# Kernel tuning notes

Measured on AMD Instinct MI355X. Metric: run time of the kernel, lower is better.

## Reference

```python
import jax, jax.numpy as jnp
import numpy as np

N = 50000   # nodes
R = 50      # relations
B = 30      # bases
F_IN = 64   # input features
H = 64      # hidden channels
C = 8       # classes
E = 1000000 # edges


def setup_inputs() -> dict:
    key = jax.random.key(0)
    ks = jax.random.split(key, 16)
    x = jax.random.normal(ks[0], (N, F_IN), jnp.float32)
    edge_index = jax.random.randint(ks[1], (2, E), 0, N)
    edge_type = jax.random.randint(ks[2], (E,), 0, R)
    inp = {"x": x, "edge_index": edge_index, "edge_type": edge_type}
    dims = [(F_IN, H), (H, H), (H, C)]
    i = 3
    for l, (din, dout) in enumerate(dims):
        s = 1.0 / np.sqrt(din)
        inp[f"bases{l}"] = jax.random.normal(ks[i], (B, din, dout), jnp.float32) * s; i += 1
        inp[f"comp{l}"] = jax.random.normal(ks[i], (R, B), jnp.float32) / np.sqrt(B); i += 1
        inp[f"root{l}"] = jax.random.normal(ks[i], (din, dout), jnp.float32) * s; i += 1
        inp[f"bias{l}"] = jnp.zeros((dout,), jnp.float32); i += 1
    return inp


def _rgcn(x, bases, comp, root, bias, src, seg):
    # Per-relation mean aggregation (PyG RGCNConv default aggr='mean'):
    # segment id = dst * R + relation. Mean of source features per (dst, rel),
    # then basis-decomposed transform (linearity lets transform follow the mean).
    din = x.shape[1]
    sums = jax.ops.segment_sum(x[src], seg, num_segments=N * R)          # [N*R, din]
    cnt = jax.ops.segment_sum(jnp.ones((seg.shape[0],), x.dtype), seg, num_segments=N * R)
    inv = jnp.where(cnt > 0, 1.0 / jnp.maximum(cnt, 1.0), 0.0)
    agg = (sums * inv[:, None]).reshape(N, R, din)                        # [N, R, din]
    t = jnp.einsum('nri,rb->nbi', agg, comp)                              # [N, B, din]
    msg = jnp.einsum('nbi,bio->no', t, bases)                             # [N, dout]
    return msg + x @ root + bias


def reference(x, edge_index, edge_type,
              bases0, comp0, root0, bias0,
              bases1, comp1, root1, bias1,
              bases2, comp2, root2, bias2):
    src, dst = edge_index[0], edge_index[1]
    seg = dst * R + edge_type
    params = [(bases0, comp0, root0, bias0),
              (bases1, comp1, root1, bias1),
              (bases2, comp2, root2, bias2)]
    x1 = x
    for b, c, r, bi in params:
        x1 = _rgcn(x, b, c, r, bi, src, seg)
        x = jax.nn.relu(x1)
    # original returns log_softmax of the last conv's pre-ReLU output
    return jax.nn.log_softmax(x1, axis=1)
```

## Files before the change

### kernel.cpp

```cpp
#include <hip/hip_runtime.h>
#include <hip/hip_bf16.h>
#include <hip/hip_fp16.h>
#include <stdint.h>

#define NN   50000
#define RR   50
#define BB   30
#define DIN  64
#define EE   1000000
#define KTOT (BB*DIN + DIN)
#define NBW  16
#define ROWE (KTOT + 8)
#define CPAD 32
#define EPAD (EE + 8*NN + 32)

typedef __attribute__((ext_vector_type(8))) short short8;
typedef __attribute__((ext_vector_type(4))) float floatx4;

#define RFL(x) __builtin_amdgcn_readfirstlane(x)


__global__ void k_hist(const int* __restrict__ dst, const int* __restrict__ et,
                       int* __restrict__ cnt) {
    int e = blockIdx.x * 256 + threadIdx.x;
    if (e < EE) {
        int d = dst[e], r = et[e];
        atomicAdd(&cnt[d * RR + r], 1);
    }
}

__global__ void k_scan1(const int* __restrict__ cnt, int* __restrict__ dcount,
                        int* __restrict__ doff, int* __restrict__ bsum) {
    __shared__ int sh[256];
    int t = threadIdx.x;
    int i = blockIdx.x * 256 + t;
    int vp = 0;
    if (i < NN) {
        const int* c = cnt + (size_t)i * RR;
        int v = 0;
#pragma unroll
        for (int r = 0; r < RR; ++r) v += c[r];
        vp = (v + 7) & ~7;
        dcount[i] = vp;
    }
    sh[t] = vp;
    __syncthreads();
    for (int s = 1; s < 256; s <<= 1) {
        int add = (t >= s) ? sh[t - s] : 0;
        __syncthreads();
        sh[t] += add;
        __syncthreads();
    }
    int incl = sh[t];
    if (i < NN) doff[i] = incl - vp;
    if (t == 255) bsum[blockIdx.x] = incl;
}

__global__ void k_scan2(int* __restrict__ bsum, int nbv) {
    __shared__ int sh[256];
    int t = threadIdx.x;
    int v = (t < nbv) ? bsum[t] : 0;
    sh[t] = v;
    __syncthreads();
    for (int s = 1; s < 256; s <<= 1) {
        int add = (t >= s) ? sh[t - s] : 0;
        __syncthreads();
        sh[t] += add;
        __syncthreads();
    }
    if (t < nbv) bsum[t] = sh[t] - v;
}

__global__ void k_scan3(int* __restrict__ doff, const int* __restrict__ bsum) {
    int i = blockIdx.x * 256 + threadIdx.x;
    if (i < NN) doff[i] += bsum[blockIdx.x];
}

__global__ void k_scatter(const int* __restrict__ src, const int* __restrict__ dst,
                          const int* __restrict__ et, const int* __restrict__ cnt,
                          const int* __restrict__ doff, int* __restrict__ cursor,
                          int2* __restrict__ ep2) {
    int e = blockIdx.x * 256 + threadIdx.x;
    if (e < EE) {
        int d = dst[e], r = et[e], s = src[e];
        int p = doff[d] + atomicAdd(&cursor[d], 1);
        float a = 1.0f / (float)cnt[d * RR + r];
        ep2[p] = make_int2(s | (r << 16), __float_as_int(a));
    }
}


__global__ void k_deghist(const int* __restrict__ dcount, int* __restrict__ dbin) {
    __shared__ int lh[256];
    int t = threadIdx.x;
    int i = blockIdx.x * 256 + t;
    lh[t] = 0;
    __syncthreads();
    if (i < NN) {
        int d = dcount[i]; d = (d > 255) ? 255 : d;
        atomicAdd(&lh[255 - d], 1);
    }
    __syncthreads();
    if (lh[t]) atomicAdd(&dbin[t], lh[t]);
}

__global__ void k_degscan(int* __restrict__ dbin) {
    __shared__ int sh[256];
    int t = threadIdx.x;
    int v = dbin[t];
    sh[t] = v;
    __syncthreads();
    for (int s = 1; s < 256; s <<= 1) {
        int add = (t >= s) ? sh[t - s] : 0;
        __syncthreads();
        sh[t] += add;
        __syncthreads();
    }
    dbin[t] = sh[t] - v;
}

__global__ void k_degscatter(const int* __restrict__ dcount, const int* __restrict__ dbin,
                             int* __restrict__ dcur, int* __restrict__ order) {
    __shared__ int lh[256], lbase[256];
    int t = threadIdx.x;
    int i = blockIdx.x * 256 + t;
    lh[t] = 0;
    __syncthreads();
    int b = 0, lpos = 0;
    if (i < NN) {
        int d = dcount[i]; d = (d > 255) ? 255 : d;
        b = 255 - d;
        lpos = atomicAdd(&lh[b], 1);
    }
    __syncthreads();
    lbase[t] = lh[t] ? atomicAdd(&dcur[t], lh[t]) : 0;
    __syncthreads();
    if (i < NN) order[dbin[b] + lbase[b] + lpos] = i;
}

__global__ void k_cast_x(const float* __restrict__ x, __hip_bfloat16* __restrict__ h) {
    int i = blockIdx.x * 256 + threadIdx.x;
    if (i < NN * DIN / 4) {
        float4 v = reinterpret_cast<const float4*>(x)[i];
        ushort4 o;
        o.x = (ushort)(__bfloat16_as_ushort(__float2bfloat16(v.x)));
        o.y = (ushort)(__bfloat16_as_ushort(__float2bfloat16(v.y)));
        o.z = (ushort)(__bfloat16_as_ushort(__float2bfloat16(v.z)));
        o.w = (ushort)(__bfloat16_as_ushort(__float2bfloat16(v.w)));
        reinterpret_cast<ushort4*>(h)[i] = o;
    }
}

__global__ void k_prep_comp3(const float* __restrict__ c0, const float* __restrict__ c1,
                             const float* __restrict__ c2, __half* __restrict__ cp) {
    int idx = blockIdx.x * 256 + threadIdx.x;
    if (idx < 3 * RR * CPAD) {
        int l = idx / (RR * CPAD);
        int rem = idx - l * (RR * CPAD);
        int r = rem / CPAD, i = rem - r * CPAD;
        const float* c = (l == 0) ? c0 : (l == 1) ? c1 : c2;
        cp[idx] = (i < BB) ? __float2half(c[r * BB + i]) : __float2half(0.f);
    }
}

__global__ void k_prep_w3(const float* __restrict__ b0, const float* __restrict__ r0,
                          const float* __restrict__ b1, const float* __restrict__ r1,
                          const float* __restrict__ b2, const float* __restrict__ r2,
                          short* __restrict__ wt) {
    int idx = blockIdx.x * 256 + threadIdx.x;
    if (idx >= 144 * KTOT) return;
    int row = idx / KTOT, k = idx - row * KTOT;
    const float* bs; const float* rt; int o, dout;
    if (row < 64)       { bs = b0; rt = r0; o = row;        dout = 64; }
    else if (row < 128) { bs = b1; rt = r1; o = row - 64;   dout = 64; }
    else                { bs = b2; rt = r2; o = row - 128;  dout = 8;  }
    float v = 0.f;
    if (o < dout)
        v = (k < BB * DIN) ? bs[k * dout + o] : rt[(k - BB * DIN) * dout + o];
    __hip_bfloat16 hb = __float2bfloat16(v);
    wt[idx] = *reinterpret_cast<const short*>(&hb);
}


#define LOADR8(u, R0, R1, R2, R3) do {                                          \
    const int _u = ((u) < nit) ? (u) : (nit - 1);                               \
    R0 = rec4[4 * _u];     R1 = rec4[4 * _u + 1];                               \
    R2 = rec4[4 * _u + 2]; R3 = rec4[4 * _u + 3];                               \
} while (0)

#define GATH1(sx) ((unsigned)xin16[((sx) & 0xFFFF) * DIN + lane])

#define EDGE_FMA1(_sx, _ai, _g) do {                                            \
    const int4* _cr = (const int4*)(compH + ((unsigned)(_sx) >> 16) * CPAD);    \
    int4 _m0 = _cr[0], _m1 = _cr[1], _m2 = _cr[2], _m3 = _cr[3];                \
    const float _xvf = __uint_as_float((unsigned)(_g) << 16) * __int_as_float(_ai); \
    const __half _xh = __float2half(_xvf);                                      \
    const __half2 _xv2 = __halves2half2(_xh, _xh);                              \
    const __half2* _p0 = reinterpret_cast<const __half2*>(&_m0);                \
    const __half2* _p1 = reinterpret_cast<const __half2*>(&_m1);                \
    const __half2* _p2 = reinterpret_cast<const __half2*>(&_m2);                \
    const __half2* _p3 = reinterpret_cast<const __half2*>(&_m3);                \
    acc[0]  = __hfma2(_p0[0], _xv2, acc[0]);                                    \
    acc[1]  = __hfma2(_p0[1], _xv2, acc[1]);                                    \
    acc[2]  = __hfma2(_p0[2], _xv2, acc[2]);                                    \
    acc[3]  = __hfma2(_p0[3], _xv2, acc[3]);                                    \
    acc[4]  = __hfma2(_p1[0], _xv2, acc[4]);                                    \
    acc[5]  = __hfma2(_p1[1], _xv2, acc[5]);                                    \
    acc[6]  = __hfma2(_p1[2], _xv2, acc[6]);                                    \
    acc[7]  = __hfma2(_p1[3], _xv2, acc[7]);                                    \
    acc[8]  = __hfma2(_p2[0], _xv2, acc[8]);                                    \
    acc[9]  = __hfma2(_p2[1], _xv2, acc[9]);                                    \
    acc[10] = __hfma2(_p2[2], _xv2, acc[10]);                                   \
    acc[11] = __hfma2(_p2[3], _xv2, acc[11]);                                   \
    acc[12] = __hfma2(_p3[0], _xv2, acc[12]);                                   \
    acc[13] = __hfma2(_p3[1], _xv2, acc[13]);                                   \
    acc[14] = __hfma2(_p3[2], _xv2, acc[14]);                                   \
    acc[15] = __hfma2(_p3[3], _xv2, acc[15]);                                   \
} while (0)

template <int DOUT, bool RELU>
__global__ __launch_bounds__(1024, 8)
void k_fused(const __hip_bfloat16* __restrict__ xin,
             const int2* __restrict__ ep2,
             const int* __restrict__ doff, const int* __restrict__ dcount,
             const int* __restrict__ order,
             const __half* __restrict__ compH,
             const short* __restrict__ Wt,
             const float* __restrict__ bias,
             void* __restrict__ outp) {
    __shared__ __align__(16) char smem_raw[NBW * ROWE * 2];
    auto t_tile = reinterpret_cast<__hip_bfloat16(*)[ROWE]>(smem_raw);
    const unsigned short* xin16 = reinterpret_cast<const unsigned short*>(xin);
    const int tid  = threadIdx.x;
    const int lane = tid & 63;
    const int wv   = RFL(tid >> 6);
    const int node0 = blockIdx.x * NBW;

    {
        const int j = wv;
        const int n = RFL(order[node0 + j]);
        __half2 acc[16];
#pragma unroll
        for (int u = 0; u < 16; ++u)
            acc[u] = __halves2half2(__float2half(0.f), __float2half(0.f));
        const int beg = RFL(doff[n]);
        const int nit = RFL(dcount[n]) >> 3;
        const unsigned selfb = (unsigned)xin16[n * DIN + lane];

        if (nit > 0) {
            const int4* rec4 = (const int4*)(ep2 + beg);
            int4 A0, A1, A2, A3, B0, B1, B2, B3, C0, C1, C2, C3;
            LOADR8(0, A0, A1, A2, A3);
            LOADR8(1, B0, B1, B2, B3);
            unsigned g0 = GATH1(RFL(A0.x)), g1 = GATH1(RFL(A0.z));
            unsigned g2 = GATH1(RFL(A1.x)), g3 = GATH1(RFL(A1.z));
            unsigned g4 = GATH1(RFL(A2.x)), g5 = GATH1(RFL(A2.z));
            unsigned g6 = GATH1(RFL(A3.x)), g7 = GATH1(RFL(A3.z));

            for (int t = 0; t < nit; ++t) {
                unsigned h0 = GATH1(RFL(B0.x)), h1 = GATH1(RFL(B0.z));
                unsigned h2 = GATH1(RFL(B1.x)), h3 = GATH1(RFL(B1.z));
                unsigned h4 = GATH1(RFL(B2.x)), h5 = GATH1(RFL(B2.z));
                unsigned h6 = GATH1(RFL(B3.x)), h7 = GATH1(RFL(B3.z));
                EDGE_FMA1(RFL(A0.x), RFL(A0.y), g0);
                EDGE_FMA1(RFL(A0.z), RFL(A0.w), g1);
                EDGE_FMA1(RFL(A1.x), RFL(A1.y), g2);
                EDGE_FMA1(RFL(A1.z), RFL(A1.w), g3);
                EDGE_FMA1(RFL(A2.x), RFL(A2.y), g4);
                EDGE_FMA1(RFL(A2.z), RFL(A2.w), g5);
                EDGE_FMA1(RFL(A3.x), RFL(A3.y), g6);
                EDGE_FMA1(RFL(A3.z), RFL(A3.w), g7);
                __builtin_amdgcn_sched_barrier(0);
                LOADR8(t + 2, C0, C1, C2, C3);
                A0 = B0; A1 = B1; A2 = B2; A3 = B3;
                B0 = C0; B1 = C1; B2 = C2; B3 = C3;
                g0 = h0; g1 = h1; g2 = h2; g3 = h3;
                g4 = h4; g5 = h5; g6 = h6; g7 = h7;
            }
        }
#pragma unroll
        for (int b = 0; b < BB; ++b) {
            const float v = (b & 1) ? __high2float(acc[b >> 1]) : __low2float(acc[b >> 1]);
            t_tile[j][b * DIN + lane] = __float2bfloat16(v);
        }
        t_tile[j][BB * DIN + lane] =
            __float2bfloat16(__uint_as_float(selfb << 16));
    }
    __syncthreads();

    const int m = lane & 15;
    const int q = lane >> 4;
    int kk0, nsteps, col_base, kpart;
    if (DOUT == 64) {
        kpart = wv >> 2;
        col_base = (wv & 3) * 16;
        kk0    = (kpart <= 1) ? kpart * 16 : (kpart == 2 ? 32 : 47);
        nsteps = (kpart <= 1) ? 16 : 15;
    } else {
        kpart = wv;
        col_base = 0;
        kk0    = (kpart < 14) ? kpart * 4 : (kpart == 14 ? 56 : 59);
        nsteps = (kpart < 14) ? 4 : 3;
    }
    const __hip_bfloat16* arow = &t_tile[m][q * 8];
    const short* brow = Wt + (size_t)(col_base + m) * KTOT + q * 8;

    floatx4 acc0 = {0.f, 0.f, 0.f, 0.f};
    floatx4 acc1 = {0.f, 0.f, 0.f, 0.f};
    int s = 0;
    for (; s + 2 <= nsteps; s += 2) {
        const int kk = kk0 + s;
        short8 a0 = *reinterpret_cast<const short8*>(arow + kk * 32);
        short8 b0 = *reinterpret_cast<const short8*>(brow + kk * 32);
        short8 a1 = *reinterpret_cast<const short8*>(arow + (kk + 1) * 32);
        short8 b1 = *reinterpret_cast<const short8*>(brow + (kk + 1) * 32);
        acc0 = __builtin_amdgcn_mfma_f32_16x16x32_bf16(a0, b0, acc0, 0, 0, 0);
        acc1 = __builtin_amdgcn_mfma_f32_16x16x32_bf16(a1, b1, acc1, 0, 0, 0);
    }
    if (s < nsteps) {
        const int kk = kk0 + s;
        short8 a0 = *reinterpret_cast<const short8*>(arow + kk * 32);
        short8 b0 = *reinterpret_cast<const short8*>(brow + kk * 32);
        acc0 = __builtin_amdgcn_mfma_f32_16x16x32_bf16(a0, b0, acc0, 0, 0, 0);
    }
    floatx4 P = acc0 + acc1;

    __syncthreads();
    float* red = (float*)smem_raw;

    if (DOUT == 64) {
        if (kpart > 0) {
            const int slot = (wv & 3) * 3 + (kpart - 1);
            const int off = (slot * 64 + lane) * 6;
            red[off] = P[0]; red[off + 1] = P[1]; red[off + 2] = P[2]; red[off + 3] = P[3];
        }
        __syncthreads();
        if (kpart == 0) {
#pragma unroll
            for (int t = 0; t < 3; ++t) {
                const int off = (((wv & 3) * 3 + t) * 64 + lane) * 6;
                P[0] += red[off]; P[1] += red[off + 1];
                P[2] += red[off + 2]; P[3] += red[off + 3];
            }
            const int o = col_base + m;
            const float bi = bias[o];
#pragma unroll
            for (int r = 0; r < 4; ++r) {
                const int n = order[node0 + q * 4 + r];
                float v = P[r] + bi;
                if (RELU) {
                    v = fmaxf(v, 0.f);
                    reinterpret_cast<__hip_bfloat16*>(outp)[(size_t)n * DOUT + o] =
                        __float2bfloat16(v);
                } else {
                    reinterpret_cast<float*>(outp)[(size_t)n * DOUT + o] = v;
                }
            }
        }
    } else {
        if (kpart > 0) {
            const int off = ((kpart - 1) * 64 + lane) * 6;
            red[off] = P[0]; red[off + 1] = P[1]; red[off + 2] = P[2]; red[off + 3] = P[3];
        }
        __syncthreads();
        if (kpart == 0) {
#pragma unroll
            for (int w = 0; w < 15; ++w) {
                const int off = (w * 64 + lane) * 6;
                P[0] += red[off]; P[1] += red[off + 1];
                P[2] += red[off + 2]; P[3] += red[off + 3];
            }
            if (m < DOUT) {
                const int o = m;
                const float bi = bias[o];
#pragma unroll
                for (int r = 0; r < 4; ++r) {
                    const int n = order[node0 + q * 4 + r];
                    reinterpret_cast<float*>(outp)[(size_t)n * DOUT + o] = P[r] + bi;
                }
            }
        }
    }
}

__global__ void k_lsm(const float* __restrict__ pre, float* __restrict__ out) {
    int n = blockIdx.x * 256 + threadIdx.x;
    if (n < NN) {
        float v[8];
        float mx = -1e30f;
#pragma unroll
        for (int c = 0; c < 8; ++c) { v[c] = pre[n * 8 + c]; mx = fmaxf(mx, v[c]); }
        float s = 0.f;
#pragma unroll
        for (int c = 0; c < 8; ++c) s += expf(v[c] - mx);
        float ls = logf(s);
#pragma unroll
        for (int c = 0; c < 8; ++c) out[n * 8 + c] = v[c] - mx - ls;
    }
}

extern "C" void kernel_launch(void* const* d_in, const int* in_sizes, int n_in,
                              void* d_out, int out_size, void* d_ws, size_t ws_size,
                              hipStream_t stream) {
    const float* x     = (const float*)d_in[0];
    const int*   eidx  = (const int*)d_in[1];
    const int*   etype = (const int*)d_in[2];
    const float* bases0 = (const float*)d_in[3];
    const float* comp0  = (const float*)d_in[4];
    const float* root0  = (const float*)d_in[5];
    const float* bias0  = (const float*)d_in[6];
    const float* bases1 = (const float*)d_in[7];
    const float* comp1  = (const float*)d_in[8];
    const float* root1  = (const float*)d_in[9];
    const float* bias1  = (const float*)d_in[10];
    const float* bases2 = (const float*)d_in[11];
    const float* comp2  = (const float*)d_in[12];
    const float* root2  = (const float*)d_in[13];
    const float* bias2  = (const float*)d_in[14];
    const int* srcp = eidx;
    const int* dstp = eidx + EE;

    char* p = (char*)d_ws;
    auto carve = [&](size_t bytes) -> char* {
        char* r = p;
        p += (bytes + 255) & ~(size_t)255;
        return r;
    };
    int*  cnt    = (int*)carve((size_t)NN * RR * sizeof(int));
    int*  dcount = (int*)carve((size_t)NN * sizeof(int));
    int*  cursor = (int*)carve((size_t)NN * sizeof(int));
    int*  doff   = (int*)carve((size_t)NN * sizeof(int));
    int*  bsum   = (int*)carve(256 * sizeof(int));
    int*  dbin   = (int*)carve(256 * sizeof(int));
    int*  dcur   = (int*)carve(256 * sizeof(int));
    int*  order  = (int*)carve((size_t)NN * sizeof(int));
    int2* ep2    = (int2*)carve((size_t)EPAD * sizeof(int2));
    __hip_bfloat16* h0 = (__hip_bfloat16*)carve((size_t)NN * DIN * 2);
    __hip_bfloat16* h1 = (__hip_bfloat16*)carve((size_t)NN * DIN * 2);
    __hip_bfloat16* h2 = (__hip_bfloat16*)carve((size_t)NN * DIN * 2);
    float* pre = (float*)carve((size_t)NN * 8 * sizeof(float));
    short* wtA = (short*)carve((size_t)144 * KTOT * sizeof(short));
    __half* cpA = (__half*)carve((size_t)3 * RR * CPAD * sizeof(__half));

    hipMemsetAsync(cnt, 0, (size_t)NN * (RR + 2) * sizeof(int) + 512, stream);
    hipMemsetAsync(dbin, 0, 2048, stream);
    hipMemsetAsync(ep2, 0, (size_t)EPAD * sizeof(int2), stream);

    const int EB = (EE + 255) / 256;
    const int NB = (NN + 255) / 256;
    k_hist<<<EB, 256, 0, stream>>>(dstp, etype, cnt);
    k_scan1<<<NB, 256, 0, stream>>>(cnt, dcount, doff, bsum);
    k_scan2<<<1, 256, 0, stream>>>(bsum, NB);
    k_scan3<<<NB, 256, 0, stream>>>(doff, bsum);
    k_scatter<<<EB, 256, 0, stream>>>(srcp, dstp, etype, cnt, doff, cursor, ep2);
    k_deghist<<<NB, 256, 0, stream>>>(dcount, dbin);
    k_degscan<<<1, 256, 0, stream>>>(dbin);
    k_degscatter<<<NB, 256, 0, stream>>>(dcount, dbin, dcur, order);
    k_cast_x<<<(NN * DIN / 4 + 255) / 256, 256, 0, stream>>>(x, h0);
    k_prep_comp3<<<(3 * RR * CPAD + 255) / 256, 256, 0, stream>>>(comp0, comp1, comp2, cpA);
    k_prep_w3<<<(144 * KTOT + 255) / 256, 256, 0, stream>>>(bases0, root0, bases1, root1,
                                                            bases2, root2, wtA);

    short* wt0 = wtA;
    short* wt1 = wtA + (size_t)64 * KTOT;
    short* wt2 = wtA + (size_t)128 * KTOT;
    __half* cp0 = cpA;
    __half* cp1 = cpA + RR * CPAD;
    __half* cp2 = cpA + 2 * RR * CPAD;

    const int NF = NN / NBW;
    k_fused<64, true ><<<NF, 1024, 0, stream>>>(h0, ep2, doff, dcount, order, cp0, wt0, bias0, (void*)h1);
    k_fused<64, true ><<<NF, 1024, 0, stream>>>(h1, ep2, doff, dcount, order, cp1, wt1, bias1, (void*)h2);
    k_fused<8,  false><<<NF, 1024, 0, stream>>>(h2, ep2, doff, dcount, order, cp2, wt2, bias2, (void*)pre);
    k_lsm<<<NB, 256, 0, stream>>>(pre, (float*)d_out);
}
```

Measured before the change: 557.0 us.

## Quantize node features to int8 with per-row scales and pack edge records

Node activations are stored as int8 with a per-node scale in place of bf16, which halves the bytes per gathered feature. Edge records shrink from 8 to 4 bytes by packing the segment count into the upper bits, with its reciprocal read from a shared-memory table. Per-edge accumulation now uses fp32 vector FMA instead of fp16 half2. The layer epilogue computes a row max through shared atomics and writes quantized outputs, which adds a synchronisation and an extra per-edge scale load, and risks accuracy loss from int8 activations.

```diff
diff --git a/kernel.cpp b/kernel.cpp
--- a/kernel.cpp
+++ b/kernel.cpp
@@ -1,6 +1,5 @@
 #include <hip/hip_runtime.h>
 #include <hip/hip_bf16.h>
-#include <hip/hip_fp16.h>
 #include <stdint.h>
 
 #define NN   50000
@@ -79,13 +78,13 @@
 __global__ void k_scatter(const int* __restrict__ src, const int* __restrict__ dst,
                           const int* __restrict__ et, const int* __restrict__ cnt,
                           const int* __restrict__ doff, int* __restrict__ cursor,
-                          int2* __restrict__ ep2) {
+                          int* __restrict__ ep) {
     int e = blockIdx.x * 256 + threadIdx.x;
     if (e < EE) {
         int d = dst[e], r = et[e], s = src[e];
         int p = doff[d] + atomicAdd(&cursor[d], 1);
-        float a = 1.0f / (float)cnt[d * RR + r];
-        ep2[p] = make_int2(s | (r << 16), __float_as_int(a));
+        int c = cnt[d * RR + r]; c = (c > 255) ? 255 : c;
+        ep[p] = s | (r << 16) | (c << 22);
     }
 }
 
@@ -138,28 +137,30 @@
     if (i < NN) order[dbin[b] + lbase[b] + lpos] = i;
 }
 
-__global__ void k_cast_x(const float* __restrict__ x, __hip_bfloat16* __restrict__ h) {
-    int i = blockIdx.x * 256 + threadIdx.x;
-    if (i < NN * DIN / 4) {
-        float4 v = reinterpret_cast<const float4*>(x)[i];
-        ushort4 o;
-        o.x = (ushort)(__bfloat16_as_ushort(__float2bfloat16(v.x)));
-        o.y = (ushort)(__bfloat16_as_ushort(__float2bfloat16(v.y)));
-        o.z = (ushort)(__bfloat16_as_ushort(__float2bfloat16(v.z)));
-        o.w = (ushort)(__bfloat16_as_ushort(__float2bfloat16(v.w)));
-        reinterpret_cast<ushort4*>(h)[i] = o;
+__global__ void k_quant_x(const float* __restrict__ x, signed char* __restrict__ xq,
+                          float* __restrict__ xs) {
+    const int wv = threadIdx.x >> 6, lane = threadIdx.x & 63;
+    const int n = blockIdx.x * 4 + wv;
+    if (n < NN) {
+        float v = x[n * DIN + lane];
+        float av = fabsf(v);
+#pragma unroll
+        for (int s = 32; s; s >>= 1) av = fmaxf(av, __shfl_xor(av, s));
+        const float inv = (av > 0.f) ? 127.f / av : 0.f;
+        xq[n * DIN + lane] = (signed char)(int)rintf(v * inv);
+        if (lane == 0) xs[n] = av * (1.f / 127.f);
     }
 }
 
 __global__ void k_prep_comp3(const float* __restrict__ c0, const float* __restrict__ c1,
-                             const float* __restrict__ c2, __half* __restrict__ cp) {
+                             const float* __restrict__ c2, float* __restrict__ cp) {
     int idx = blockIdx.x * 256 + threadIdx.x;
     if (idx < 3 * RR * CPAD) {
         int l = idx / (RR * CPAD);
         int rem = idx - l * (RR * CPAD);
         int r = rem / CPAD, i = rem - r * CPAD;
         const float* c = (l == 0) ? c0 : (l == 1) ? c1 : c2;
-        cp[idx] = (i < BB) ? __float2half(c[r * BB + i]) : __float2half(0.f);
+        cp[idx] = (i < BB) ? c[r * BB + i] : 0.f;
     }
 }
 
@@ -182,109 +183,91 @@
 }
 
 
-#define LOADR8(u, R0, R1, R2, R3) do {                                          \
+#define LOADR8(u, RA, RB) do {                                                  \
     const int _u = ((u) < nit) ? (u) : (nit - 1);                               \
-    R0 = rec4[4 * _u];     R1 = rec4[4 * _u + 1];                               \
-    R2 = rec4[4 * _u + 2]; R3 = rec4[4 * _u + 3];                               \
+    RA = rec4[2 * _u]; RB = rec4[2 * _u + 1];                                   \
 } while (0)
 
-#define GATH1(sx) ((unsigned)xin16[((sx) & 0xFFFF) * DIN + lane])
-
-#define EDGE_FMA1(_sx, _ai, _g) do {                                            \
-    const int4* _cr = (const int4*)(compH + ((unsigned)(_sx) >> 16) * CPAD);    \
-    int4 _m0 = _cr[0], _m1 = _cr[1], _m2 = _cr[2], _m3 = _cr[3];                \
-    const float _xvf = __uint_as_float((unsigned)(_g) << 16) * __int_as_float(_ai); \
-    const __half _xh = __float2half(_xvf);                                      \
-    const __half2 _xv2 = __halves2half2(_xh, _xh);                              \
-    const __half2* _p0 = reinterpret_cast<const __half2*>(&_m0);                \
-    const __half2* _p1 = reinterpret_cast<const __half2*>(&_m1);                \
-    const __half2* _p2 = reinterpret_cast<const __half2*>(&_m2);                \
-    const __half2* _p3 = reinterpret_cast<const __half2*>(&_m3);                \
-    acc[0]  = __hfma2(_p0[0], _xv2, acc[0]);                                    \
-    acc[1]  = __hfma2(_p0[1], _xv2, acc[1]);                                    \
-    acc[2]  = __hfma2(_p0[2], _xv2, acc[2]);                                    \
-    acc[3]  = __hfma2(_p0[3], _xv2, acc[3]);                                    \
-    acc[4]  = __hfma2(_p1[0], _xv2, acc[4]);                                    \
-    acc[5]  = __hfma2(_p1[1], _xv2, acc[5]);                                    \
-    acc[6]  = __hfma2(_p1[2], _xv2, acc[6]);                                    \
-    acc[7]  = __hfma2(_p1[3], _xv2, acc[7]);                                    \
-    acc[8]  = __hfma2(_p2[0], _xv2, acc[8]);                                    \
-    acc[9]  = __hfma2(_p2[1], _xv2, acc[9]);                                    \
-    acc[10] = __hfma2(_p2[2], _xv2, acc[10]);                                   \
-    acc[11] = __hfma2(_p2[3], _xv2, acc[11]);                                   \
-    acc[12] = __hfma2(_p3[0], _xv2, acc[12]);                                   \
-    acc[13] = __hfma2(_p3[1], _xv2, acc[13]);                                   \
-    acc[14] = __hfma2(_p3[2], _xv2, acc[14]);                                   \
-    acc[15] = __hfma2(_p3[3], _xv2, acc[15]);                                   \
+#define GATH1(sx) ((int)xss[((sx) & 0xFFFF) * DIN + lane])
+
+#define EDGE_FMA1(_sx, _gi) do {                                                \
+    const int _c = ((_sx) >> 22) & 255;                                         \
+    const float _sc = xscale[(_sx) & 0xFFFF];                                   \
+    const float _a = _sc * rcpl[_c];                                            \
+    const floatx4* _q = (const floatx4*)(compP + (((_sx) >> 16) & 63) * CPAD);  \
+    const float _xv = (float)(_gi) * _a;                                        \
+    const floatx4 _w = {_xv, _xv, _xv, _xv};                                    \
+    acc[0] = _q[0] * _w + acc[0];  acc[1] = _q[1] * _w + acc[1];                \
+    acc[2] = _q[2] * _w + acc[2];  acc[3] = _q[3] * _w + acc[3];                \
+    acc[4] = _q[4] * _w + acc[4];  acc[5] = _q[5] * _w + acc[5];                \
+    acc[6] = _q[6] * _w + acc[6];  acc[7] = _q[7] * _w + acc[7];                \
 } while (0)
 
 template <int DOUT, bool RELU>
 __global__ __launch_bounds__(1024, 8)
-void k_fused(const __hip_bfloat16* __restrict__ xin,
-             const int2* __restrict__ ep2,
+void k_fused(const signed char* __restrict__ xss,
+             const float* __restrict__ xscale,
+             const int* __restrict__ ep,
              const int* __restrict__ doff, const int* __restrict__ dcount,
              const int* __restrict__ order,
-             const __half* __restrict__ compH,
+             const float* __restrict__ compP,
              const short* __restrict__ Wt,
              const float* __restrict__ bias,
-             void* __restrict__ outp) {
+             void* __restrict__ outp,
+             float* __restrict__ oscale) {
     __shared__ __align__(16) char smem_raw[NBW * ROWE * 2];
+    __shared__ float rcpl[256];
     auto t_tile = reinterpret_cast<__hip_bfloat16(*)[ROWE]>(smem_raw);
-    const unsigned short* xin16 = reinterpret_cast<const unsigned short*>(xin);
     const int tid  = threadIdx.x;
     const int lane = tid & 63;
     const int wv   = RFL(tid >> 6);
     const int node0 = blockIdx.x * NBW;
 
+    if (tid < 256) rcpl[tid] = (tid == 0) ? 0.f : (1.0f / (float)tid);
+
+    const int n   = RFL(order[node0 + wv]);
+    const int beg = RFL(doff[n]);
+    const int nit = RFL(dcount[n]) >> 3;
+    const int selfq = GATH1(n);
+    const float sscale = RFL(__float_as_int(xscale[n])) == 0 ? 0.f : xscale[n];
+
+    __syncthreads();
+
     {
-        const int j = wv;
-        const int n = RFL(order[node0 + j]);
-        __half2 acc[16];
-#pragma unroll
-        for (int u = 0; u < 16; ++u)
-            acc[u] = __halves2half2(__float2half(0.f), __float2half(0.f));
-        const int beg = RFL(doff[n]);
-        const int nit = RFL(dcount[n]) >> 3;
-        const unsigned selfb = (unsigned)xin16[n * DIN + lane];
+        floatx4 acc[8];
+#pragma unroll
+        for (int u = 0; u < 8; ++u) acc[u] = (floatx4){0.f, 0.f, 0.f, 0.f};
 
         if (nit > 0) {
-            const int4* rec4 = (const int4*)(ep2 + beg);
-            int4 A0, A1, A2, A3, B0, B1, B2, B3, C0, C1, C2, C3;
-            LOADR8(0, A0, A1, A2, A3);
-            LOADR8(1, B0, B1, B2, B3);
-            unsigned g0 = GATH1(RFL(A0.x)), g1 = GATH1(RFL(A0.z));
-            unsigned g2 = GATH1(RFL(A1.x)), g3 = GATH1(RFL(A1.z));
-            unsigned g4 = GATH1(RFL(A2.x)), g5 = GATH1(RFL(A2.z));
-            unsigned g6 = GATH1(RFL(A3.x)), g7 = GATH1(RFL(A3.z));
+            const int4* rec4 = (const int4*)(ep + beg);
+            int4 A0, A1, B0, B1, C0, C1;
+            LOADR8(0, A0, A1);
+            LOADR8(1, B0, B1);
+            int g0 = GATH1(RFL(A0.x)), g1 = GATH1(RFL(A0.y));
+            int g2 = GATH1(RFL(A0.z)), g3 = GATH1(RFL(A0.w));
+            int g4 = GATH1(RFL(A1.x)), g5 = GATH1(RFL(A1.y));
+            int g6 = GATH1(RFL(A1.z)), g7 = GATH1(RFL(A1.w));
 
             for (int t = 0; t < nit; ++t) {
-                unsigned h0 = GATH1(RFL(B0.x)), h1 = GATH1(RFL(B0.z));
-                unsigned h2 = GATH1(RFL(B1.x)), h3 = GATH1(RFL(B1.z));
-                unsigned h4 = GATH1(RFL(B2.x)), h5 = GATH1(RFL(B2.z));
-                unsigned h6 = GATH1(RFL(B3.x)), h7 = GATH1(RFL(B3.z));
-                EDGE_FMA1(RFL(A0.x), RFL(A0.y), g0);
-                EDGE_FMA1(RFL(A0.z), RFL(A0.w), g1);
-                EDGE_FMA1(RFL(A1.x), RFL(A1.y), g2);
-                EDGE_FMA1(RFL(A1.z), RFL(A1.w), g3);
-                EDGE_FMA1(RFL(A2.x), RFL(A2.y), g4);
-                EDGE_FMA1(RFL(A2.z), RFL(A2.w), g5);
-                EDGE_FMA1(RFL(A3.x), RFL(A3.y), g6);
-                EDGE_FMA1(RFL(A3.z), RFL(A3.w), g7);
+                int h0 = GATH1(RFL(B0.x)), h1 = GATH1(RFL(B0.y));
+                int h2 = GATH1(RFL(B0.z)), h3 = GATH1(RFL(B0.w));
+                int h4 = GATH1(RFL(B1.x)), h5 = GATH1(RFL(B1.y));
+                int h6 = GATH1(RFL(B1.z)), h7 = GATH1(RFL(B1.w));
+                EDGE_FMA1(RFL(A0.x), g0); EDGE_FMA1(RFL(A0.y), g1);
+                EDGE_FMA1(RFL(A0.z), g2); EDGE_FMA1(RFL(A0.w), g3);
+                EDGE_FMA1(RFL(A1.x), g4); EDGE_FMA1(RFL(A1.y), g5);
+                EDGE_FMA1(RFL(A1.z), g6); EDGE_FMA1(RFL(A1.w), g7);
                 __builtin_amdgcn_sched_barrier(0);
-                LOADR8(t + 2, C0, C1, C2, C3);
-                A0 = B0; A1 = B1; A2 = B2; A3 = B3;
-                B0 = C0; B1 = C1; B2 = C2; B3 = C3;
+                LOADR8(t + 2, C0, C1);
+                A0 = B0; A1 = B1; B0 = C0; B1 = C1;
                 g0 = h0; g1 = h1; g2 = h2; g3 = h3;
                 g4 = h4; g5 = h5; g6 = h6; g7 = h7;
             }
         }
 #pragma unroll
-        for (int b = 0; b < BB; ++b) {
-            const float v = (b & 1) ? __high2float(acc[b >> 1]) : __low2float(acc[b >> 1]);
-            t_tile[j][b * DIN + lane] = __float2bfloat16(v);
-        }
-        t_tile[j][BB * DIN + lane] =
-            __float2bfloat16(__uint_as_float(selfb << 16));
+        for (int b = 0; b < BB; ++b)
+            t_tile[wv][b * DIN + lane] = __float2bfloat16(acc[b >> 2][b & 3]);
+        t_tile[wv][BB * DIN + lane] = __float2bfloat16((float)selfq * sscale);
     }
     __syncthreads();
 
@@ -327,6 +310,7 @@
 
     __syncthreads();
     float* red = (float*)smem_raw;
+    float* rowmax = (float*)(smem_raw + 20480);
 
     if (DOUT == 64) {
         if (kpart > 0) {
@@ -334,7 +318,9 @@
             const int off = (slot * 64 + lane) * 6;
             red[off] = P[0]; red[off + 1] = P[1]; red[off + 2] = P[2]; red[off + 3] = P[3];
         }
-        __syncthreads();
+        if (tid < 16) ((int*)rowmax)[tid] = 0;
+        __syncthreads();
+        float vr[4];
         if (kpart == 0) {
 #pragma unroll
             for (int t = 0; t < 3; ++t) {
@@ -346,15 +332,23 @@
             const float bi = bias[o];
 #pragma unroll
             for (int r = 0; r < 4; ++r) {
-                const int n = order[node0 + q * 4 + r];
-                float v = P[r] + bi;
-                if (RELU) {
-                    v = fmaxf(v, 0.f);
-                    reinterpret_cast<__hip_bfloat16*>(outp)[(size_t)n * DOUT + o] =
-                        __float2bfloat16(v);
-                } else {
-                    reinterpret_cast<float*>(outp)[(size_t)n * DOUT + o] = v;
-                }
+                const float v = fmaxf(P[r] + bi, 0.f);
+                vr[r] = v;
+                atomicMax((int*)&rowmax[q * 4 + r], __float_as_int(v));
+            }
+        }
+        __syncthreads();
+        if (kpart == 0) {
+            const int o = col_base + m;
+#pragma unroll
+            for (int r = 0; r < 4; ++r) {
+                const int slot2 = q * 4 + r;
+                const float mx = rowmax[slot2];
+                const float inv = (mx > 0.f) ? 127.f / mx : 0.f;
+                const int nw = order[node0 + slot2];
+                reinterpret_cast<signed char*>(outp)[(size_t)nw * 64 + o] =
+                    (signed char)(int)rintf(vr[r] * inv);
+                if (wv == 0 && m == 0) oscale[nw] = mx * (1.f / 127.f);
             }
         }
     } else {
@@ -375,8 +369,8 @@
                 const float bi = bias[o];
 #pragma unroll
                 for (int r = 0; r < 4; ++r) {
-                    const int n = order[node0 + q * 4 + r];
-                    reinterpret_cast<float*>(outp)[(size_t)n * DOUT + o] = P[r] + bi;
+                    const int nw = order[node0 + q * 4 + r];
+                    reinterpret_cast<float*>(outp)[(size_t)nw * DOUT + o] = P[r] + bi;
                 }
             }
         }
@@ -434,17 +428,18 @@
     int*  dbin   = (int*)carve(256 * sizeof(int));
     int*  dcur   = (int*)carve(256 * sizeof(int));
     int*  order  = (int*)carve((size_t)NN * sizeof(int));
-    int2* ep2    = (int2*)carve((size_t)EPAD * sizeof(int2));
-    __hip_bfloat16* h0 = (__hip_bfloat16*)carve((size_t)NN * DIN * 2);
-    __hip_bfloat16* h1 = (__hip_bfloat16*)carve((size_t)NN * DIN * 2);
-    __hip_bfloat16* h2 = (__hip_bfloat16*)carve((size_t)NN * DIN * 2);
+    int*  ep     = (int*)carve((size_t)EPAD * sizeof(int));
+    signed char* xqA = (signed char*)carve((size_t)NN * DIN);
+    signed char* xqB = (signed char*)carve((size_t)NN * DIN);
+    float* xsA = (float*)carve((size_t)NN * sizeof(float));
+    float* xsB = (float*)carve((size_t)NN * sizeof(float));
     float* pre = (float*)carve((size_t)NN * 8 * sizeof(float));
     short* wtA = (short*)carve((size_t)144 * KTOT * sizeof(short));
-    __half* cpA = (__half*)carve((size_t)3 * RR * CPAD * sizeof(__half));
+    float* cpA = (float*)carve((size_t)3 * RR * CPAD * sizeof(float));
 
     hipMemsetAsync(cnt, 0, (size_t)NN * (RR + 2) * sizeof(int) + 512, stream);
     hipMemsetAsync(dbin, 0, 2048, stream);
-    hipMemsetAsync(ep2, 0, (size_t)EPAD * sizeof(int2), stream);
+    hipMemsetAsync(ep, 0, (size_t)EPAD * sizeof(int), stream);
 
     const int EB = (EE + 255) / 256;
     const int NB = (NN + 255) / 256;
@@ -452,11 +447,11 @@
     k_scan1<<<NB, 256, 0, stream>>>(cnt, dcount, doff, bsum);
     k_scan2<<<1, 256, 0, stream>>>(bsum, NB);
     k_scan3<<<NB, 256, 0, stream>>>(doff, bsum);
-    k_scatter<<<EB, 256, 0, stream>>>(srcp, dstp, etype, cnt, doff, cursor, ep2);
+    k_scatter<<<EB, 256, 0, stream>>>(srcp, dstp, etype, cnt, doff, cursor, ep);
     k_deghist<<<NB, 256, 0, stream>>>(dcount, dbin);
     k_degscan<<<1, 256, 0, stream>>>(dbin);
     k_degscatter<<<NB, 256, 0, stream>>>(dcount, dbin, dcur, order);
-    k_cast_x<<<(NN * DIN / 4 + 255) / 256, 256, 0, stream>>>(x, h0);
+    k_quant_x<<<(NN + 3) / 4, 256, 0, stream>>>(x, xqA, xsA);
     k_prep_comp3<<<(3 * RR * CPAD + 255) / 256, 256, 0, stream>>>(comp0, comp1, comp2, cpA);
     k_prep_w3<<<(144 * KTOT + 255) / 256, 256, 0, stream>>>(bases0, root0, bases1, root1,
                                                             bases2, root2, wtA);
@@ -464,13 +459,16 @@
     short* wt0 = wtA;
     short* wt1 = wtA + (size_t)64 * KTOT;
     short* wt2 = wtA + (size_t)128 * KTOT;
-    __half* cp0 = cpA;
-    __half* cp1 = cpA + RR * CPAD;
-    __half* cp2 = cpA + 2 * RR * CPAD;
+    float* cp0 = cpA;
+    float* cp1 = cpA + RR * CPAD;
+    float* cp2 = cpA + 2 * RR * CPAD;
 
     const int NF = NN / NBW;
-    k_fused<64, true ><<<NF, 1024, 0, stream>>>(h0, ep2, doff, dcount, order, cp0, wt0, bias0, (void*)h1);
-    k_fused<64, true ><<<NF, 1024, 0, stream>>>(h1, ep2, doff, dcount, order, cp1, wt1, bias1, (void*)h2);
-    k_fused<8,  false><<<NF, 1024, 0, stream>>>(h2, ep2, doff, dcount, order, cp2, wt2, bias2, (void*)pre);
+    k_fused<64, true ><<<NF, 1024, 0, stream>>>(xqA, xsA, ep, doff, dcount, order,
+                                                cp0, wt0, bias0, (void*)xqB, xsB);
+    k_fused<64, true ><<<NF, 1024, 0, stream>>>(xqB, xsB, ep, doff, dcount, order,
+                                                cp1, wt1, bias1, (void*)xqA, xsA);
+    k_fused<8,  false><<<NF, 1024, 0, stream>>>(xqA, xsA, ep, doff, dcount, order,
+                                                cp2, wt2, bias2, (void*)pre, xsB);
     k_lsm<<<NB, 256, 0, stream>>>(pre, (float*)d_out);
 }
```

Result: slower. 615.7 us (+10.5%).
